# Kernel tuning notes

Measured on AMD Instinct MI355X. Metric: run time of the kernel, lower is better.

## Reference

```python
import jax, jax.numpy as jnp
import numpy as np

FEATURE_LEN = 64
DIM_ATOM = 256
DIM_GRAPH = 256
NUM_NEI = 32
B = 2048          # reactions / graphs in batch
ATOMS = 30        # atoms per molecule graph
N = B * ATOMS     # total nodes
E = 4 * N         # total edges
NMOL = 100000     # knowledge-graph molecule table size
S = 2             # molecules per reaction side (len(id_list))


def setup_inputs() -> dict:
    key = jax.random.key(0)
    ks = jax.random.split(key, 16)
    xavier = lambda k, shape: (jax.random.normal(k, shape, jnp.float32)
                               * np.sqrt(2.0 / (shape[0] + shape[-1])))
    return {
        "node_feat": jax.random.randint(ks[0], (N, 4), 0, FEATURE_LEN, jnp.int32),
        "edge_src": jax.random.randint(ks[1], (E,), 0, N, jnp.int32),
        "edge_dst": jax.random.randint(ks[2], (E,), 0, N, jnp.int32),
        "graph_ids": jnp.repeat(jnp.arange(B, dtype=jnp.int32), ATOMS),
        "id_list": jax.random.randint(ks[3], (S, B), 0, NMOL, jnp.int32),
        "id_list_target": jax.random.randint(ks[4], (S, B), 0, NMOL, jnp.int32),
        "all_mfea": (jax.random.uniform(ks[5], (NMOL, 40)) < 0.3).astype(jnp.float32),
        "neighbor_matrix": jax.random.randint(ks[6], (NMOL, NUM_NEI), 0, NMOL, jnp.int32),
        "W0": xavier(ks[7], (FEATURE_LEN, DIM_ATOM)),
        "b0": jnp.zeros((DIM_ATOM,), jnp.float32),
        "W1": xavier(ks[8], (DIM_ATOM, DIM_ATOM)),
        "b1": jnp.zeros((DIM_ATOM,), jnp.float32),
        "fea_emb": xavier(ks[9], (40, DIM_GRAPH)),
        "att_w": xavier(ks[10], (DIM_GRAPH, 1)),
        "att_b": jnp.zeros((1,), jnp.float32),
        "crosscl_w": xavier(ks[11], (DIM_GRAPH, DIM_ATOM)),
        "crosscl_b": jnp.zeros((DIM_ATOM,), jnp.float32),
    }


def reference(node_feat, edge_src, edge_dst, graph_ids, id_list, id_list_target,
              all_mfea, neighbor_matrix,
              W0, b0, W1, b1, fea_emb, att_w, att_b, crosscl_w, crosscl_b):
    n = node_feat.shape[0]
    # --- atom-level GCN (DGL GraphConv, norm='both') ---
    h = jax.nn.one_hot(node_feat, FEATURE_LEN, dtype=jnp.float32).sum(axis=1)  # [N, F]
    ones_e = jnp.ones((edge_src.shape[0],), jnp.float32)
    deg_out = jnp.clip(jax.ops.segment_sum(ones_e, edge_src, n), 1.0)
    deg_in = jnp.clip(jax.ops.segment_sum(ones_e, edge_dst, n), 1.0)
    norm_src = deg_out[:, None] ** -0.5
    norm_dst = deg_in[:, None] ** -0.5

    def gcn(x, W, b, act):
        m = (x * norm_src)[edge_src]                        # gather along edges
        agg = jax.ops.segment_sum(m, edge_dst, n)           # scatter-add
        z = (agg * norm_dst) @ W + b
        return act(z)

    h = gcn(h, W0, b0, jax.nn.relu)
    h = gcn(h, W1, b1, lambda z: z)
    # factor computed via python float() in torch -> detached constant
    factor = np.sqrt(DIM_ATOM).astype(np.float32) / jax.lax.stop_gradient(
        jnp.mean(jnp.linalg.norm(h, axis=1)))
    h = h * factor
    mol_atom_embedding = jax.ops.segment_sum(h, graph_ids, B)  # SumPooling [B, D]

    # --- reaction-level KG aggregation ---
    src_emb = jnp.einsum('sbf,fg->sbg', all_mfea[id_list], fea_emb)         # [S,B,G]
    tgt_emb = jnp.einsum('sbf,fg->sbg', all_mfea[id_list_target], fea_emb)  # [S,B,G]
    source_re = src_emb.mean(axis=0)   # 1/len * sum
    target_re = tgt_emb.mean(axis=0)

    item_emb = src_emb                                       # [S,B,G]
    nei_idx = neighbor_matrix[id_list]                       # [S,B,K]
    nei_emb = jnp.einsum('sbkf,fg->sbkg', all_mfea[nei_idx], fea_emb)  # [S,B,K,G]

    target_embedding = source_re + target_re                 # [B,G]
    score_nei = item_emb[:, :, None, :] * nei_emb * target_embedding[None, :, None, :]
    logits = score_nei @ att_w + att_b                       # [S,B,K,1]
    score_att = jax.nn.softmax(logits, axis=2)
    nei_agg = jnp.sum(score_att * nei_emb, axis=2)           # [S,B,G]

    mol_reaction_embedding = (item_emb + nei_agg).mean(axis=0)  # [B,G]
    mol_x_embedding = mol_reaction_embedding @ crosscl_w + crosscl_b
    mol_embedding = jnp.concatenate([mol_atom_embedding, mol_reaction_embedding], axis=1)
    return mol_embedding, mol_atom_embedding, mol_x_embedding
```

## Files before the change

### kernel.cpp

```cpp
#include <hip/hip_runtime.h>
#include <math.h>

#define N_NODES 61440
#define N_EDGES 245760
#define BATCH   2048
#define ATOMS   30
#define F_LEN   64
#define DIM     256
#define NUM_NEI 32
#define MF      40
#define ECAP    512

typedef __attribute__((ext_vector_type(8))) short s8v;
typedef __attribute__((ext_vector_type(4))) float f4v;

__device__ __forceinline__ unsigned short f2bf(float x) {
    union { float f; unsigned u; } c; c.f = x;
    unsigned r = (c.u + 0x7FFFu + ((c.u >> 16) & 1u)) >> 16;
    return (unsigned short)r;
}
__device__ __forceinline__ float bf2f(unsigned short u) {
    union { unsigned u; float f; } c; c.u = ((unsigned)u) << 16;
    return c.f;
}

__global__ void k_deg(const int* __restrict__ esrc, const int* __restrict__ edst,
                      int* deg_out, int* deg_in) {
    int e = blockIdx.x * 256 + threadIdx.x;
    if (e < N_EDGES) {
        atomicAdd(&deg_out[esrc[e]], 1);
        atomicAdd(&deg_in[edst[e]], 1);
    }
}

__global__ void k_alloc(const int* __restrict__ deg_in, int* row_start, int* cursor,
                        int* counter) {
    int t = threadIdx.x;
    int n = blockIdx.x * 256 + t;
    int lane = t & 63;
    int d = deg_in[n];
    int p = d;
#pragma unroll
    for (int o = 1; o < 64; o <<= 1) { int v = __shfl_up(p, o, 64); if (lane >= o) p += v; }
    int base = 0;
    if (lane == 63) base = atomicAdd(counter, p);
    base = __shfl(base, 63, 64);
    int v = base + p - d;
    row_start[n] = v;
    cursor[n] = v;
}

__global__ void k_csr_fill(const int* __restrict__ esrc, const int* __restrict__ edst,
                           int* cursor, int* csr_src) {
    int e = blockIdx.x * 256 + threadIdx.x;
    if (e < N_EDGES) {
        int p = atomicAdd(&cursor[edst[e]], 1);
        csr_src[p] = esrc[e];
    }
}

__global__ void k_prepw(const float* __restrict__ W0, const float* __restrict__ W1,
                        unsigned short* w0bt, unsigned short* w1bt) {
    int n = blockIdx.x, k = threadIdx.x;
    w1bt[(size_t)n * 256 + k] = f2bf(W1[(size_t)k * 256 + n]);
    if (k < 64) w0bt[(size_t)n * 64 + k] = f2bf(W0[(size_t)k * 256 + n]);
}

__global__ __launch_bounds__(256) void k_gcn0(
    const int* __restrict__ nf, const int* __restrict__ row_start,
    const int* __restrict__ csr_src, const int* __restrict__ deg_in,
    const int* __restrict__ deg_out, const unsigned short* __restrict__ w0bt,
    const float* __restrict__ b0, unsigned short* __restrict__ h1b) {
    __shared__ float la0[32 * 68];
    __shared__ int4  enf[ECAP];
    __shared__ float ens[ECAP];
    __shared__ int   rs[33];
    __shared__ float lnd[32], lns[32];
    __shared__ float b0c[256];
    int n0 = blockIdx.x * 32;
    int t = threadIdx.x;
    if (t < 32) rs[t] = row_start[n0 + t];
    if (t == 0) rs[32] = row_start[n0 + 31] + deg_in[n0 + 31];
    if (t < 32) {
        lnd[t] = rsqrtf((float)max(deg_in[n0 + t], 1));
        lns[t] = rsqrtf((float)max(deg_out[n0 + t], 1));
    }
    b0c[t] = b0[t];
    __syncthreads();
    int beg0 = rs[0];
    int tot = rs[32] - beg0; if (tot > ECAP) tot = ECAP;
    for (int e = t; e < tot; e += 256) {
        int s = csr_src[beg0 + e];
        enf[e] = ((const int4*)nf)[s];
        ens[e] = rsqrtf((float)max(deg_out[s], 1));
    }
    __syncthreads();
    {
        int row = t >> 3, kc = (t & 7) * 8;
        float a[8];
#pragma unroll
        for (int j = 0; j < 8; j++) a[j] = 0.f;
        int lo = rs[row] - beg0, hi = rs[row + 1] - beg0;
        if (hi > tot) hi = tot;
        for (int e = lo; e < hi; e++) {
            int4 f = enf[e]; float w = ens[e];
#pragma unroll
            for (int j = 0; j < 8; j++) {
                int k = kc + j;
                a[j] += w * (float)((f.x == k) + (f.y == k) + (f.z == k) + (f.w == k));
            }
        }
#pragma unroll
        for (int j = 0; j < 8; j++) la0[row * 68 + kc + j] = a[j];
    }
    __syncthreads();
    int lane = t & 63, wv = t >> 6;
    int ln = lane & 15, lg = lane >> 4;
    f4v acc[2][4];
#pragma unroll
    for (int mi = 0; mi < 2; mi++)
#pragma unroll
        for (int ni = 0; ni < 4; ni++) acc[mi][ni] = (f4v)0.f;
#pragma unroll
    for (int kst = 0; kst < 2; kst++) {
        s8v afr[2];
#pragma unroll
        for (int mi = 0; mi < 2; mi++) {
            const float* p = &la0[(mi * 16 + ln) * 68 + kst * 32 + lg * 8];
            f4v lo = *(const f4v*)p;
            f4v hi = *(const f4v*)(p + 4);
            s8v a;
#pragma unroll
            for (int j = 0; j < 4; j++) { a[j] = (short)f2bf(lo[j]); a[4 + j] = (short)f2bf(hi[j]); }
            afr[mi] = a;
        }
#pragma unroll
        for (int ni = 0; ni < 4; ni++) {
            int n = wv * 64 + ni * 16 + ln;
            s8v b = *(const s8v*)&w0bt[(size_t)n * 64 + kst * 32 + lg * 8];
            acc[0][ni] = __builtin_amdgcn_mfma_f32_16x16x32_bf16(afr[0], b, acc[0][ni], 0, 0, 0);
            acc[1][ni] = __builtin_amdgcn_mfma_f32_16x16x32_bf16(afr[1], b, acc[1][ni], 0, 0, 0);
        }
    }
#pragma unroll
    for (int mi = 0; mi < 2; mi++)
#pragma unroll
        for (int ni = 0; ni < 4; ni++) {
            int n = wv * 64 + ni * 16 + ln;
            float bb = b0c[n];
#pragma unroll
            for (int r = 0; r < 4; r++) {
                int m = mi * 16 + lg * 4 + r;
                float z = acc[mi][ni][r] * lnd[m] + bb;
                z = fmaxf(z, 0.f) * lns[m];
                h1b[(size_t)(n0 + m) * 256 + n] = f2bf(z);
            }
        }
}

__global__ __launch_bounds__(256) void k_gcn1(
    const unsigned short* __restrict__ h1b, const int* __restrict__ row_start,
    const int* __restrict__ csr_src, const int* __restrict__ deg_in,
    const unsigned short* __restrict__ w1bt, const float* __restrict__ b1,
    unsigned short* __restrict__ h2b, float* __restrict__ partial) {
    __shared__ unsigned short lab[32 * 264];
    __shared__ int   ecache[ECAP];
    __shared__ int   rs[33];
    __shared__ float lnd[32];
    __shared__ float b1c[256];
    __shared__ float nsq[32];
    int n0 = blockIdx.x * 32;
    int t = threadIdx.x;
    if (t < 32) rs[t] = row_start[n0 + t];
    if (t == 0) rs[32] = row_start[n0 + 31] + deg_in[n0 + 31];
    if (t < 32) {
        lnd[t] = rsqrtf((float)max(deg_in[n0 + t], 1));
        nsq[t] = 0.f;
    }
    b1c[t] = b1[t];
    __syncthreads();
    int beg0 = rs[0];
    int tot = rs[32] - beg0; if (tot > ECAP) tot = ECAP;
    for (int e = t; e < tot; e += 256) ecache[e] = csr_src[beg0 + e];
    __syncthreads();
    {
        int gr = t >> 5;
        int gc = (t & 31) * 8;
        int lo[4], hi[4];
#pragma unroll
        for (int r = 0; r < 4; r++) {
            int i = gr + r * 8;
            lo[r] = rs[i] - beg0;
            hi[r] = rs[i + 1] - beg0;
            if (hi[r] > tot) hi[r] = tot;
        }
        float a[4][8];
#pragma unroll
        for (int r = 0; r < 4; r++)
#pragma unroll
            for (int j = 0; j < 8; j++) a[r][j] = 0.f;
        int mx = 0;
#pragma unroll
        for (int r = 0; r < 4; r++) mx = max(mx, hi[r] - lo[r]);
        for (int it = 0; it < mx; ++it) {
#pragma unroll
            for (int r = 0; r < 4; r++) {
                int e = lo[r] + it;
                if (e < hi[r]) {
                    int s = ecache[e];
                    s8v v = *(const s8v*)&h1b[(size_t)s * 256 + gc];
#pragma unroll
                    for (int j = 0; j < 8; j++) a[r][j] += bf2f((unsigned short)v[j]);
                }
            }
        }
#pragma unroll
        for (int r = 0; r < 4; r++) {
            int i = gr + r * 8;
            s8v ov;
#pragma unroll
            for (int j = 0; j < 8; j++) ov[j] = (short)f2bf(a[r][j]);
            *(s8v*)&lab[i * 264 + gc] = ov;
        }
    }
    __syncthreads();
    int lane = t & 63, wv = t >> 6;
    int ln = lane & 15, lg = lane >> 4;
    f4v acc[2][4];
#pragma unroll
    for (int mi = 0; mi < 2; mi++)
#pragma unroll
        for (int ni = 0; ni < 4; ni++) acc[mi][ni] = (f4v)0.f;
#pragma unroll 2
    for (int kst = 0; kst < 8; kst++) {
        s8v afr[2];
#pragma unroll
        for (int mi = 0; mi < 2; mi++)
            afr[mi] = *(const s8v*)&lab[(mi * 16 + ln) * 264 + kst * 32 + lg * 8];
#pragma unroll
        for (int ni = 0; ni < 4; ni++) {
            int n = wv * 64 + ni * 16 + ln;
            s8v b = *(const s8v*)&w1bt[(size_t)n * 256 + kst * 32 + lg * 8];
            acc[0][ni] = __builtin_amdgcn_mfma_f32_16x16x32_bf16(afr[0], b, acc[0][ni], 0, 0, 0);
            acc[1][ni] = __builtin_amdgcn_mfma_f32_16x16x32_bf16(afr[1], b, acc[1][ni], 0, 0, 0);
        }
    }
    float sm[2][4];
#pragma unroll
    for (int mi = 0; mi < 2; mi++)
#pragma unroll
        for (int r = 0; r < 4; r++) sm[mi][r] = 0.f;
#pragma unroll
    for (int mi = 0; mi < 2; mi++)
#pragma unroll
        for (int ni = 0; ni < 4; ni++) {
            int n = wv * 64 + ni * 16 + ln;
            float bb = b1c[n];
#pragma unroll
            for (int r = 0; r < 4; r++) {
                int m = mi * 16 + lg * 4 + r;
                float z = acc[mi][ni][r] * lnd[m] + bb;
                h2b[(size_t)(n0 + m) * 256 + n] = f2bf(z);
                sm[mi][r] += z * z;
            }
        }
#pragma unroll
    for (int mi = 0; mi < 2; mi++)
#pragma unroll
        for (int r = 0; r < 4; r++) {
            float v = sm[mi][r];
            v += __shfl_xor(v, 1);
            v += __shfl_xor(v, 2);
            v += __shfl_xor(v, 4);
            v += __shfl_xor(v, 8);
            if (ln == 0) atomicAdd(&nsq[mi * 16 + lg * 4 + r], v);
        }
    __syncthreads();
    if (t < 32) atomicAdd(&partial[(n0 + t) & 1023], sqrtf(nsq[t]));
}

__global__ void k_normfin(const float* __restrict__ partial, float* factor) {
    __shared__ float red[256];
    int t = threadIdx.x;
    float s = partial[t] + partial[t + 256] + partial[t + 512] + partial[t + 768];
    red[t] = s;
    __syncthreads();
    for (int o = 128; o; o >>= 1) {
        if (t < o) red[t] += red[t + o];
        __syncthreads();
    }
    if (t == 0) factor[0] = 16.0f / (red[0] / (float)N_NODES);
}

__global__ void k_pool(const unsigned short* __restrict__ h2b,
                       const float* __restrict__ factor, float* out) {
    int b = blockIdx.x, t = threadIdx.x;
    float fac = factor[0];
    float s = 0.f;
    for (int a = 0; a < ATOMS; a++) s += bf2f(h2b[(size_t)(b * ATOMS + a) * DIM + t]);
    s *= fac;
    out[(size_t)b * 512 + t] = s;
    out[(size_t)BATCH * 512 + (size_t)b * DIM + t] = s;
}

__global__ __launch_bounds__(256) void k_rxn(
    const int* __restrict__ id_list, const int* __restrict__ id_list_t,
    const int* __restrict__ neimat, const float* __restrict__ mfea,
    const float* __restrict__ fea_emb, const float* __restrict__ att_w,
    const float* __restrict__ att_b, const float* __restrict__ crosscl_w,
    const float* __restrict__ crosscl_b, float* __restrict__ out) {
    __shared__ float com[MF];
    __shared__ float mitem[MF];
    __shared__ float u[DIM];
    __shared__ float nm[NUM_NEI * MF];
    __shared__ float vv[MF];
    __shared__ float aw[NUM_NEI];
    __shared__ float mre[DIM];
    int b = blockIdx.x;
    int t = threadIdx.x;
    int wv = t >> 6, lane = t & 63;
    if (t < MF) {
        int i0 = id_list[b], i1 = id_list[BATCH + b];
        int j0 = id_list_t[b], j1 = id_list_t[BATCH + b];
        com[t] = 0.5f * (mfea[(size_t)i0 * MF + t] + mfea[(size_t)i1 * MF + t])
               + 0.5f * (mfea[(size_t)j0 * MF + t] + mfea[(size_t)j1 * MF + t]);
    }
    __syncthreads();
    float tg = 0.f;
    for (int f = 0; f < MF; f++) tg += com[f] * fea_emb[f * DIM + t];
    float awt = att_w[t];
    float msum = 0.f;
    for (int s = 0; s < 2; s++) {
        int id = id_list[s * BATCH + b];
        __syncthreads();
        if (t < MF) mitem[t] = mfea[(size_t)id * MF + t];
        for (int i = t; i < NUM_NEI * MF; i += 256) {
            int k = i / MF, f = i - k * MF;
            int nid = neimat[(size_t)id * NUM_NEI + k];
            nm[i] = mfea[(size_t)nid * MF + f];
        }
        __syncthreads();
        float item = 0.f;
        for (int f = 0; f < MF; f++) item += mitem[f] * fea_emb[f * DIM + t];
        u[t] = item * tg * awt;
        __syncthreads();
        for (int i = 0; i < 5; i++) {
            int f = wv + 8 * i;
            float p = 0.f;
#pragma unroll
            for (int j = 0; j < 4; j++) p += u[lane + 64 * j] * fea_emb[f * DIM + lane + 64 * j];
#pragma unroll
            for (int off = 32; off; off >>= 1) p += __shfl_down(p, off, 64);
            if (lane == 0) vv[f] = p;
        }
        __syncthreads();
        if (wv == 0) {
            float lg = -1e30f;
            if (lane < NUM_NEI) {
                lg = att_b[0];
                for (int f = 0; f < MF; f++) lg += nm[lane * MF + f] * vv[f];
            }
            float m = lg;
#pragma unroll
            for (int off = 16; off; off >>= 1) m = fmaxf(m, __shfl_xor(m, off, 32));
            float e = (lane < NUM_NEI) ? __expf(lg - m) : 0.f;
            float ssum = e;
#pragma unroll
            for (int off = 16; off; off >>= 1) ssum += __shfl_xor(ssum, off, 32);
            if (lane < NUM_NEI) aw[lane] = e / ssum;
        }
        __syncthreads();
        if (t < MF) {
            float w = 0.f;
            for (int k = 0; k < NUM_NEI; k++) w += aw[k] * nm[k * MF + t];
            vv[t] = w;
        }
        __syncthreads();
        float na = 0.f;
        for (int f = 0; f < MF; f++) na += vv[f] * fea_emb[f * DIM + t];
        msum += item + na;
    }
    float m = 0.5f * msum;
    out[(size_t)b * 512 + DIM + t] = m;
    mre[t] = m;
    __syncthreads();
    float acc = crosscl_b[t];
    for (int uu = 0; uu < DIM; uu++) acc += mre[uu] * crosscl_w[uu * DIM + t];
    out[(size_t)BATCH * 768 + (size_t)b * DIM + t] = acc;
}

extern "C" void kernel_launch(void* const* d_in, const int* in_sizes, int n_in,
                              void* d_out, int out_size, void* d_ws, size_t ws_size,
                              hipStream_t stream) {
    const int*   node_feat = (const int*)d_in[0];
    const int*   edge_src  = (const int*)d_in[1];
    const int*   edge_dst  = (const int*)d_in[2];
    const int*   id_list   = (const int*)d_in[4];
    const int*   id_list_t = (const int*)d_in[5];
    const float* all_mfea  = (const float*)d_in[6];
    const int*   neimat    = (const int*)d_in[7];
    const float* W0        = (const float*)d_in[8];
    const float* b0        = (const float*)d_in[9];
    const float* W1        = (const float*)d_in[10];
    const float* b1        = (const float*)d_in[11];
    const float* fea_emb   = (const float*)d_in[12];
    const float* att_w     = (const float*)d_in[13];
    const float* att_b     = (const float*)d_in[14];
    const float* crosscl_w = (const float*)d_in[15];
    const float* crosscl_b = (const float*)d_in[16];
    float* out = (float*)d_out;

    char* ws = (char*)d_ws;
    int*   deg_out   = (int*)ws;            ws += (size_t)N_NODES * 4;
    int*   deg_in    = (int*)ws;            ws += (size_t)N_NODES * 4;
    float* partial   = (float*)ws;          ws += 1024 * 4;
    float* factor    = (float*)ws;
    int*   counter   = (int*)(ws + 8);      ws += 256;
    int*   row_start = (int*)ws;            ws += (size_t)N_NODES * 4;
    int*   cursor    = (int*)ws;            ws += (size_t)N_NODES * 4;
    int*   csr_srcb  = (int*)ws;            ws += (size_t)N_EDGES * 4;
    unsigned short* w0bt = (unsigned short*)ws; ws += (size_t)256 * 64 * 2;
    unsigned short* w1bt = (unsigned short*)ws; ws += (size_t)256 * 256 * 2;
    unsigned short* h1b  = (unsigned short*)ws; ws += (size_t)N_NODES * DIM * 2;
    unsigned short* h2b  = (unsigned short*)ws; ws += (size_t)N_NODES * DIM * 2;

    hipMemsetAsync(deg_out, 0, (size_t)N_NODES * 8 + 1024 * 4 + 256, stream);

    k_deg<<<(N_EDGES + 255) / 256, 256, 0, stream>>>(edge_src, edge_dst, deg_out, deg_in);
    k_alloc<<<N_NODES / 256, 256, 0, stream>>>(deg_in, row_start, cursor, counter);
    k_csr_fill<<<(N_EDGES + 255) / 256, 256, 0, stream>>>(edge_src, edge_dst, cursor, csr_srcb);
    k_prepw<<<256, 256, 0, stream>>>(W0, W1, w0bt, w1bt);

    k_gcn0<<<N_NODES / 32, 256, 0, stream>>>(node_feat, row_start, csr_srcb, deg_in,
                                             deg_out, w0bt, b0, h1b);
    k_gcn1<<<N_NODES / 32, 256, 0, stream>>>(h1b, row_start, csr_srcb, deg_in,
                                             w1bt, b1, h2b, partial);
    k_normfin<<<1, 256, 0, stream>>>(partial, factor);
    k_pool<<<BATCH, 256, 0, stream>>>(h2b, factor, out);
    k_rxn<<<BATCH, 256, 0, stream>>>(id_list, id_list_t, neimat, all_mfea, fea_emb,
                                     att_w, att_b, crosscl_w, crosscl_b, out);
}
```

Measured before the change: 194.3 us.

## Fuse graph pooling into GCN layer-2 epilogue via atomics; unroll gather loop

The second GCN kernel no longer writes the full bf16 node feature matrix. Its epilogue atomically accumulates each node's output into a per-graph pooled buffer indexed by graph_ids, and the separate pooling kernel is removed, with scaling folded into the reaction kernel. The neighbor-gather loop is also restructured to issue two predicated loads per row per iteration for more memory-level parallelism. In exchange it adds many global float atomics (32 nodes x 256 columns per block, into about 2 graphs) and a larger memset, and the pooled sums become fp32 and order-nondeterministic.

```diff
diff --git a/kernel.cpp b/kernel.cpp
--- a/kernel.cpp
+++ b/kernel.cpp
@@ -161,14 +161,16 @@
 __global__ __launch_bounds__(256) void k_gcn1(
     const unsigned short* __restrict__ h1b, const int* __restrict__ row_start,
     const int* __restrict__ csr_src, const int* __restrict__ deg_in,
+    const int* __restrict__ graph_ids,
     const unsigned short* __restrict__ w1bt, const float* __restrict__ b1,
-    unsigned short* __restrict__ h2b, float* __restrict__ partial) {
+    float* __restrict__ pooled, float* __restrict__ partial) {
     __shared__ unsigned short lab[32 * 264];
     __shared__ int   ecache[ECAP];
     __shared__ int   rs[33];
     __shared__ float lnd[32];
     __shared__ float b1c[256];
     __shared__ float nsq[32];
+    __shared__ int   gid[32];
     int n0 = blockIdx.x * 32;
     int t = threadIdx.x;
     if (t < 32) rs[t] = row_start[n0 + t];
@@ -176,6 +178,7 @@
     if (t < 32) {
         lnd[t] = rsqrtf((float)max(deg_in[n0 + t], 1));
         nsq[t] = 0.f;
+        gid[t] = graph_ids[n0 + t];
     }
     b1c[t] = b1[t];
     __syncthreads();
@@ -186,33 +189,43 @@
     {
         int gr = t >> 5;
         int gc = (t & 31) * 8;
-        int lo[4], hi[4];
+        int lo[4], cnt[4];
 #pragma unroll
         for (int r = 0; r < 4; r++) {
             int i = gr + r * 8;
             lo[r] = rs[i] - beg0;
-            hi[r] = rs[i + 1] - beg0;
-            if (hi[r] > tot) hi[r] = tot;
+            int h = rs[i + 1] - beg0; if (h > tot) h = tot;
+            cnt[r] = h - lo[r];
         }
         float a[4][8];
 #pragma unroll
         for (int r = 0; r < 4; r++)
 #pragma unroll
             for (int j = 0; j < 8; j++) a[r][j] = 0.f;
-        int mx = 0;
-#pragma unroll
-        for (int r = 0; r < 4; r++) mx = max(mx, hi[r] - lo[r]);
-        for (int it = 0; it < mx; ++it) {
-#pragma unroll
-            for (int r = 0; r < 4; r++) {
-                int e = lo[r] + it;
-                if (e < hi[r]) {
-                    int s = ecache[e];
-                    s8v v = *(const s8v*)&h1b[(size_t)s * 256 + gc];
-#pragma unroll
-                    for (int j = 0; j < 8; j++) a[r][j] += bf2f((unsigned short)v[j]);
+        int mx = max(max(cnt[0], cnt[1]), max(cnt[2], cnt[3]));
+        for (int it = 0; it < mx; it += 2) {
+            int sidx[4][2]; float wm[4][2];
+#pragma unroll
+            for (int r = 0; r < 4; r++)
+#pragma unroll
+                for (int u = 0; u < 2; u++) {
+                    bool val = (it + u) < cnt[r];
+                    sidx[r][u] = ecache[val ? (lo[r] + it + u) : 0];
+                    wm[r][u] = val ? 1.f : 0.f;
                 }
-            }
+            s8v v[4][2];
+#pragma unroll
+            for (int r = 0; r < 4; r++)
+#pragma unroll
+                for (int u = 0; u < 2; u++)
+                    v[r][u] = *(const s8v*)&h1b[(size_t)sidx[r][u] * 256 + gc];
+#pragma unroll
+            for (int r = 0; r < 4; r++)
+#pragma unroll
+                for (int u = 0; u < 2; u++)
+#pragma unroll
+                    for (int j = 0; j < 8; j++)
+                        a[r][j] = fmaf(wm[r][u], bf2f((unsigned short)v[r][u][j]), a[r][j]);
         }
 #pragma unroll
         for (int r = 0; r < 4; r++) {
@@ -260,7 +273,7 @@
             for (int r = 0; r < 4; r++) {
                 int m = mi * 16 + lg * 4 + r;
                 float z = acc[mi][ni][r] * lnd[m] + bb;
-                h2b[(size_t)(n0 + m) * 256 + n] = f2bf(z);
+                atomicAdd(&pooled[(size_t)gid[m] * 256 + n], z);
                 sm[mi][r] += z * z;
             }
         }
@@ -292,23 +305,13 @@
     if (t == 0) factor[0] = 16.0f / (red[0] / (float)N_NODES);
 }
 
-__global__ void k_pool(const unsigned short* __restrict__ h2b,
-                       const float* __restrict__ factor, float* out) {
-    int b = blockIdx.x, t = threadIdx.x;
-    float fac = factor[0];
-    float s = 0.f;
-    for (int a = 0; a < ATOMS; a++) s += bf2f(h2b[(size_t)(b * ATOMS + a) * DIM + t]);
-    s *= fac;
-    out[(size_t)b * 512 + t] = s;
-    out[(size_t)BATCH * 512 + (size_t)b * DIM + t] = s;
-}
-
 __global__ __launch_bounds__(256) void k_rxn(
     const int* __restrict__ id_list, const int* __restrict__ id_list_t,
     const int* __restrict__ neimat, const float* __restrict__ mfea,
     const float* __restrict__ fea_emb, const float* __restrict__ att_w,
     const float* __restrict__ att_b, const float* __restrict__ crosscl_w,
-    const float* __restrict__ crosscl_b, float* __restrict__ out) {
+    const float* __restrict__ crosscl_b, const float* __restrict__ pooled,
+    const float* __restrict__ factor, float* __restrict__ out) {
     __shared__ float com[MF];
     __shared__ float mitem[MF];
     __shared__ float u[DIM];
@@ -319,6 +322,9 @@
     int b = blockIdx.x;
     int t = threadIdx.x;
     int wv = t >> 6, lane = t & 63;
+    float pv = pooled[(size_t)b * 256 + t] * factor[0];
+    out[(size_t)b * 512 + t] = pv;
+    out[(size_t)BATCH * 512 + (size_t)b * DIM + t] = pv;
     if (t < MF) {
         int i0 = id_list[b], i1 = id_list[BATCH + b];
         int j0 = id_list_t[b], j1 = id_list_t[BATCH + b];
@@ -395,6 +401,7 @@
     const int*   node_feat = (const int*)d_in[0];
     const int*   edge_src  = (const int*)d_in[1];
     const int*   edge_dst  = (const int*)d_in[2];
+    const int*   graph_ids = (const int*)d_in[3];
     const int*   id_list   = (const int*)d_in[4];
     const int*   id_list_t = (const int*)d_in[5];
     const float* all_mfea  = (const float*)d_in[6];
@@ -411,20 +418,22 @@
     float* out = (float*)d_out;
 
     char* ws = (char*)d_ws;
+    char* zbase = ws;
     int*   deg_out   = (int*)ws;            ws += (size_t)N_NODES * 4;
     int*   deg_in    = (int*)ws;            ws += (size_t)N_NODES * 4;
     float* partial   = (float*)ws;          ws += 1024 * 4;
     float* factor    = (float*)ws;
     int*   counter   = (int*)(ws + 8);      ws += 256;
+    float* pooled    = (float*)ws;          ws += (size_t)BATCH * 256 * 4;
+    size_t zbytes = (size_t)(ws - zbase);
     int*   row_start = (int*)ws;            ws += (size_t)N_NODES * 4;
     int*   cursor    = (int*)ws;            ws += (size_t)N_NODES * 4;
     int*   csr_srcb  = (int*)ws;            ws += (size_t)N_EDGES * 4;
     unsigned short* w0bt = (unsigned short*)ws; ws += (size_t)256 * 64 * 2;
     unsigned short* w1bt = (unsigned short*)ws; ws += (size_t)256 * 256 * 2;
     unsigned short* h1b  = (unsigned short*)ws; ws += (size_t)N_NODES * DIM * 2;
-    unsigned short* h2b  = (unsigned short*)ws; ws += (size_t)N_NODES * DIM * 2;
-
-    hipMemsetAsync(deg_out, 0, (size_t)N_NODES * 8 + 1024 * 4 + 256, stream);
+
+    hipMemsetAsync(zbase, 0, zbytes, stream);
 
     k_deg<<<(N_EDGES + 255) / 256, 256, 0, stream>>>(edge_src, edge_dst, deg_out, deg_in);
     k_alloc<<<N_NODES / 256, 256, 0, stream>>>(deg_in, row_start, cursor, counter);
@@ -433,10 +442,10 @@
 
     k_gcn0<<<N_NODES / 32, 256, 0, stream>>>(node_feat, row_start, csr_srcb, deg_in,
                                              deg_out, w0bt, b0, h1b);
-    k_gcn1<<<N_NODES / 32, 256, 0, stream>>>(h1b, row_start, csr_srcb, deg_in,
-                                             w1bt, b1, h2b, partial);
+    k_gcn1<<<N_NODES / 32, 256, 0, stream>>>(h1b, row_start, csr_srcb, deg_in, graph_ids,
+                                             w1bt, b1, pooled, partial);
     k_normfin<<<1, 256, 0, stream>>>(partial, factor);
-    k_pool<<<BATCH, 256, 0, stream>>>(h2b, factor, out);
     k_rxn<<<BATCH, 256, 0, stream>>>(id_list, id_list_t, neimat, all_mfea, fea_emb,
-                                     att_w, att_b, crosscl_w, crosscl_b, out);
-}
+                                     att_w, att_b, crosscl_w, crosscl_b, pooled,
+                                     factor, out);
+}
```

Result: slower. 342.7 us (+76.3%).

## Stage neighbor gathers via direct global-to-LDS loads in gcn1; fuse pooling into rxn

Applied to the files above, without the earlier changes.

The neighbor aggregation in k_gcn1 now processes edges in chunks of 64. Each wave issues global_load_lds to copy whole 512-byte source rows into a shared staging buffer, and threads then accumulate their rows from LDS instead of issuing scattered per-thread global loads. The graph pooling kernel is removed and its work folded into the start of k_rxn, which saves one launch and one pass. This costs 32KB of extra LDS per block, which may lower occupancy, plus extra barriers per chunk.

```diff
diff --git a/kernel.cpp b/kernel.cpp
--- a/kernel.cpp
+++ b/kernel.cpp
@@ -10,9 +10,12 @@
 #define NUM_NEI 32
 #define MF      40
 #define ECAP    512
+#define CHUNK   64
 
 typedef __attribute__((ext_vector_type(8))) short s8v;
 typedef __attribute__((ext_vector_type(4))) float f4v;
+typedef __attribute__((address_space(3))) unsigned lds_u32;
+typedef const __attribute__((address_space(1))) unsigned glb_u32;
 
 __device__ __forceinline__ unsigned short f2bf(float x) {
     union { float f; unsigned u; } c; c.f = x;
@@ -163,6 +166,7 @@
     const int* __restrict__ csr_src, const int* __restrict__ deg_in,
     const unsigned short* __restrict__ w1bt, const float* __restrict__ b1,
     unsigned short* __restrict__ h2b, float* __restrict__ partial) {
+    __shared__ unsigned short stage[CHUNK * 256];
     __shared__ unsigned short lab[32 * 264];
     __shared__ int   ecache[ECAP];
     __shared__ int   rs[33];
@@ -171,6 +175,7 @@
     __shared__ float nsq[32];
     int n0 = blockIdx.x * 32;
     int t = threadIdx.x;
+    int lane = t & 63, wv = t >> 6;
     if (t < 32) rs[t] = row_start[n0 + t];
     if (t == 0) rs[32] = row_start[n0 + 31] + deg_in[n0 + 31];
     if (t < 32) {
@@ -183,48 +188,57 @@
     int tot = rs[32] - beg0; if (tot > ECAP) tot = ECAP;
     for (int e = t; e < tot; e += 256) ecache[e] = csr_src[beg0 + e];
     __syncthreads();
-    {
-        int gr = t >> 5;
-        int gc = (t & 31) * 8;
-        int lo[4], hi[4];
+    int gr = t >> 5;
+    int gc = (t & 31) * 8;
+    int lo[4], hi[4];
+#pragma unroll
+    for (int r = 0; r < 4; r++) {
+        int i = gr + r * 8;
+        lo[r] = rs[i] - beg0;
+        int h = rs[i + 1] - beg0; if (h > tot) h = tot;
+        hi[r] = h;
+    }
+    float a[4][8];
+#pragma unroll
+    for (int r = 0; r < 4; r++)
+#pragma unroll
+        for (int j = 0; j < 8; j++) a[r][j] = 0.f;
+    int lhalf = (lane >> 5) & 1;
+    for (int c0 = 0; c0 < tot; c0 += CHUNK) {
+        int nch = min(CHUNK, tot - c0);
+        int npair = (nch + 1) >> 1;
+        for (int p = wv; p < npair; p += 4) {
+            int e = c0 + 2 * p + lhalf;
+            int ecl = min(e, tot - 1);
+            int sv = ecache[ecl];
+            const unsigned short* src = h1b + (size_t)sv * 256 + (lane & 31) * 8;
+            __builtin_amdgcn_global_load_lds((glb_u32*)src,
+                                             (lds_u32*)&stage[(size_t)(2 * p) * 256],
+                                             16, 0, 0);
+        }
+        asm volatile("s_waitcnt vmcnt(0)" ::: "memory");
+        __syncthreads();
 #pragma unroll
         for (int r = 0; r < 4; r++) {
-            int i = gr + r * 8;
-            lo[r] = rs[i] - beg0;
-            hi[r] = rs[i + 1] - beg0;
-            if (hi[r] > tot) hi[r] = tot;
-        }
-        float a[4][8];
-#pragma unroll
-        for (int r = 0; r < 4; r++)
-#pragma unroll
-            for (int j = 0; j < 8; j++) a[r][j] = 0.f;
-        int mx = 0;
-#pragma unroll
-        for (int r = 0; r < 4; r++) mx = max(mx, hi[r] - lo[r]);
-        for (int it = 0; it < mx; ++it) {
-#pragma unroll
-            for (int r = 0; r < 4; r++) {
-                int e = lo[r] + it;
-                if (e < hi[r]) {
-                    int s = ecache[e];
-                    s8v v = *(const s8v*)&h1b[(size_t)s * 256 + gc];
-#pragma unroll
-                    for (int j = 0; j < 8; j++) a[r][j] += bf2f((unsigned short)v[j]);
-                }
+            int es = max(lo[r], c0) - c0;
+            int ee = min(hi[r], c0 + nch) - c0;
+            for (int e = es; e < ee; e++) {
+                s8v v = *(const s8v*)&stage[e * 256 + gc];
+#pragma unroll
+                for (int j = 0; j < 8; j++) a[r][j] += bf2f((unsigned short)v[j]);
             }
         }
-#pragma unroll
-        for (int r = 0; r < 4; r++) {
-            int i = gr + r * 8;
-            s8v ov;
-#pragma unroll
-            for (int j = 0; j < 8; j++) ov[j] = (short)f2bf(a[r][j]);
-            *(s8v*)&lab[i * 264 + gc] = ov;
-        }
-    }
-    __syncthreads();
-    int lane = t & 63, wv = t >> 6;
+        __syncthreads();
+    }
+#pragma unroll
+    for (int r = 0; r < 4; r++) {
+        int i = gr + r * 8;
+        s8v ov;
+#pragma unroll
+        for (int j = 0; j < 8; j++) ov[j] = (short)f2bf(a[r][j]);
+        *(s8v*)&lab[i * 264 + gc] = ov;
+    }
+    __syncthreads();
     int ln = lane & 15, lg = lane >> 4;
     f4v acc[2][4];
 #pragma unroll
@@ -292,23 +306,13 @@
     if (t == 0) factor[0] = 16.0f / (red[0] / (float)N_NODES);
 }
 
-__global__ void k_pool(const unsigned short* __restrict__ h2b,
-                       const float* __restrict__ factor, float* out) {
-    int b = blockIdx.x, t = threadIdx.x;
-    float fac = factor[0];
-    float s = 0.f;
-    for (int a = 0; a < ATOMS; a++) s += bf2f(h2b[(size_t)(b * ATOMS + a) * DIM + t]);
-    s *= fac;
-    out[(size_t)b * 512 + t] = s;
-    out[(size_t)BATCH * 512 + (size_t)b * DIM + t] = s;
-}
-
 __global__ __launch_bounds__(256) void k_rxn(
     const int* __restrict__ id_list, const int* __restrict__ id_list_t,
     const int* __restrict__ neimat, const float* __restrict__ mfea,
     const float* __restrict__ fea_emb, const float* __restrict__ att_w,
     const float* __restrict__ att_b, const float* __restrict__ crosscl_w,
-    const float* __restrict__ crosscl_b, float* __restrict__ out) {
+    const float* __restrict__ crosscl_b, const unsigned short* __restrict__ h2b,
+    const float* __restrict__ factor, float* __restrict__ out) {
     __shared__ float com[MF];
     __shared__ float mitem[MF];
     __shared__ float u[DIM];
@@ -319,6 +323,11 @@
     int b = blockIdx.x;
     int t = threadIdx.x;
     int wv = t >> 6, lane = t & 63;
+    float pv = 0.f;
+    for (int a = 0; a < ATOMS; a++) pv += bf2f(h2b[(size_t)(b * ATOMS + a) * DIM + t]);
+    pv *= factor[0];
+    out[(size_t)b * 512 + t] = pv;
+    out[(size_t)BATCH * 512 + (size_t)b * DIM + t] = pv;
     if (t < MF) {
         int i0 = id_list[b], i1 = id_list[BATCH + b];
         int j0 = id_list_t[b], j1 = id_list_t[BATCH + b];
@@ -411,11 +420,13 @@
     float* out = (float*)d_out;
 
     char* ws = (char*)d_ws;
+    char* zbase = ws;
     int*   deg_out   = (int*)ws;            ws += (size_t)N_NODES * 4;
     int*   deg_in    = (int*)ws;            ws += (size_t)N_NODES * 4;
     float* partial   = (float*)ws;          ws += 1024 * 4;
     float* factor    = (float*)ws;
     int*   counter   = (int*)(ws + 8);      ws += 256;
+    size_t zbytes = (size_t)(ws - zbase);
     int*   row_start = (int*)ws;            ws += (size_t)N_NODES * 4;
     int*   cursor    = (int*)ws;            ws += (size_t)N_NODES * 4;
     int*   csr_srcb  = (int*)ws;            ws += (size_t)N_EDGES * 4;
@@ -424,7 +435,7 @@
     unsigned short* h1b  = (unsigned short*)ws; ws += (size_t)N_NODES * DIM * 2;
     unsigned short* h2b  = (unsigned short*)ws; ws += (size_t)N_NODES * DIM * 2;
 
-    hipMemsetAsync(deg_out, 0, (size_t)N_NODES * 8 + 1024 * 4 + 256, stream);
+    hipMemsetAsync(zbase, 0, zbytes, stream);
 
     k_deg<<<(N_EDGES + 255) / 256, 256, 0, stream>>>(edge_src, edge_dst, deg_out, deg_in);
     k_alloc<<<N_NODES / 256, 256, 0, stream>>>(deg_in, row_start, cursor, counter);
@@ -436,7 +447,7 @@
     k_gcn1<<<N_NODES / 32, 256, 0, stream>>>(h1b, row_start, csr_srcb, deg_in,
                                              w1bt, b1, h2b, partial);
     k_normfin<<<1, 256, 0, stream>>>(partial, factor);
-    k_pool<<<BATCH, 256, 0, stream>>>(h2b, factor, out);
     k_rxn<<<BATCH, 256, 0, stream>>>(id_list, id_list_t, neimat, all_mfea, fea_emb,
-                                     att_w, att_b, crosscl_w, crosscl_b, out);
-}
+                                     att_w, att_b, crosscl_w, crosscl_b, h2b,
+                                     factor, out);
+}
```

Result: no change. 191.0 us (-1.7%).
